# Optimization experiments

Measured on AMD Instinct MI355X. Metric: run time of the kernel, lower is better.

## Reference

```python
import jax, jax.numpy as jnp
import numpy as np

NUM_LEVELS = 4
RADIUS = 3
B, H, W, C = 2, 64, 64, 64
N = 4096


def _bilinear_sample(feat, coords):
    # feat: (B, H, W, C); coords: (B, N, 2) in [0,W-1]x[0,H-1]
    Bf, Hf, Wf, Cf = feat.shape
    x = coords[..., 0]
    y = coords[..., 1]
    x0 = jnp.clip(jnp.floor(x).astype(jnp.int32), 0, Wf - 1)
    x1 = jnp.clip(jnp.floor(x).astype(jnp.int32) + 1, 0, Wf - 1)
    y0 = jnp.clip(jnp.floor(y).astype(jnp.int32), 0, Hf - 1)
    y1 = jnp.clip(jnp.floor(y).astype(jnp.int32) + 1, 0, Hf - 1)
    # weights use the CLIPPED corner coords (matches original code order)
    wa = (x1.astype(jnp.float32) - x) * (y1.astype(jnp.float32) - y)
    wb = (x1.astype(jnp.float32) - x) * (y - y0.astype(jnp.float32))
    wc = (x - x0.astype(jnp.float32)) * (y1.astype(jnp.float32) - y)
    wd = (x - x0.astype(jnp.float32)) * (y - y0.astype(jnp.float32))
    bidx = jnp.arange(Bf)[:, None]
    Ia = feat[bidx, y0, x0, :]
    Ib = feat[bidx, y1, x0, :]
    Ic = feat[bidx, y0, x1, :]
    Id = feat[bidx, y1, x1, :]
    return (wa[..., None] * Ia + wb[..., None] * Ib
            + wc[..., None] * Ic + wd[..., None] * Id)


def _build_pyramid(fmap2):
    # pyramid holds L2-normalized fmap2 at successively halved resolutions
    f = fmap2 / (jnp.linalg.norm(fmap2, axis=-1, keepdims=True) + 1e-6)
    pyr = [f]
    cur = f
    for level in range(NUM_LEVELS - 1):
        cur = jax.image.resize(
            cur, (B, H // 2 ** (level + 1), W // 2 ** (level + 1), C),
            method='bilinear')
        pyr.append(cur)
    return pyr


def _corr_block(fmap1, fmap2, coords):
    r = RADIUS
    # fmap1 is normalized in the original but its result is unused; replicate faithfully
    _ = fmap1 / (jnp.linalg.norm(fmap1, axis=-1, keepdims=True) + 1e-6)
    pyramid = _build_pyramid(fmap2)
    # (dx, dy) offsets, dy outer / dx inner to match original concat order
    offsets = jnp.array([[dx, dy] for dy in range(-r, r + 1)
                         for dx in range(-r, r + 1)], dtype=jnp.float32)  # (K,2)
    K = offsets.shape[0]
    outs = []
    for level, corr in enumerate(pyramid):
        scale = 2 ** level
        H_l, W_l = corr.shape[1], corr.shape[2]
        coords_scaled = coords / scale                       # (B,N,2)
        coords_off = coords_scaled[None] + offsets[:, None, None, :]  # (K,B,N,2)
        coords_off = jnp.clip(coords_off,
                              jnp.array([0.0, 0.0]),
                              jnp.array([W_l - 1, H_l - 1], dtype=jnp.float32))
        sampled = jax.vmap(_bilinear_sample, in_axes=(None, 0))(corr, coords_off)  # (K,B,N,C)
        outs.append(jnp.moveaxis(sampled, 0, 2).reshape(coords.shape[0], coords.shape[1], K * corr.shape[-1]))
    return jnp.concatenate(outs, axis=-1)  # (B, N, NUM_LEVELS*K*C)


def setup_inputs() -> dict:
    key = jax.random.key(0)
    k1, k2, k3 = jax.random.split(key, 3)
    fmap1 = jax.random.normal(k1, (B, H, W, C), dtype=jnp.float32)
    fmap2 = jax.random.normal(k2, (B, H, W, C), dtype=jnp.float32)
    coords = jax.random.uniform(k3, (B, N, 2), dtype=jnp.float32) \
        * jnp.array([W - 1, H - 1], dtype=jnp.float32)
    return {"fmap1": fmap1, "fmap2": fmap2, "coords": coords}


def reference(fmap1, fmap2, coords):
    return _corr_block(fmap1, fmap2, coords)
```

## Files before the change

### kernel.cpp

```cpp
#include <hip/hip_runtime.h>
#include <math.h>


__global__ __launch_bounds__(256) void normalize_kernel(
    const float* __restrict__ in, float* __restrict__ out) {
  int gtid = blockIdx.x * 256 + threadIdx.x;
  int wave = gtid >> 6;
  int lane = gtid & 63;
  float v = in[wave * 64 + lane];
  float ss = v * v;
  #pragma unroll
  for (int m = 32; m >= 1; m >>= 1) ss += __shfl_xor(ss, m);
  out[wave * 64 + lane] = v / (sqrtf(ss) + 1e-6f);
}

__global__ __launch_bounds__(256) void downsample_kernel(
    const float* __restrict__ in, float* __restrict__ out, int Si) {
  int So = Si >> 1;
  int gtid = blockIdx.x * 256 + threadIdx.x;
  int wave = gtid >> 6;
  int lane = gtid & 63;
  int ox = wave % So;
  int t  = wave / So;
  int oy = t % So;
  int b  = t / So;

  int xs[4], ys[4];
  float wx[4], wy[4];
  float bw[4] = {0.25f, 0.75f, 0.75f, 0.25f};
  float sx = 0.f, sy = 0.f;
  #pragma unroll
  for (int tt = 0; tt < 4; tt++) {
    int jx = 2 * ox - 1 + tt;
    bool vx = (jx >= 0) && (jx < Si);
    xs[tt] = vx ? jx : 0;
    wx[tt] = vx ? bw[tt] : 0.f;
    sx += wx[tt];
    int jy = 2 * oy - 1 + tt;
    bool vy = (jy >= 0) && (jy < Si);
    ys[tt] = vy ? jy : 0;
    wy[tt] = vy ? bw[tt] : 0.f;
    sy += wy[tt];
  }
  float ix = 1.f / sx, iy = 1.f / sy;
  #pragma unroll
  for (int tt = 0; tt < 4; tt++) { wx[tt] *= ix; wy[tt] *= iy; }

  float acc = 0.f;
  #pragma unroll
  for (int a = 0; a < 4; a++) {
    const float* rp = in + ((long)(b * Si + ys[a]) * Si) * 64 + lane;
    float row = 0.f;
    #pragma unroll
    for (int tt = 0; tt < 4; tt++) row += wx[tt] * rp[xs[tt] * 64];
    acc += wy[a] * row;
  }
  out[((long)(b * So + oy) * So + ox) * 64 + lane] = acc;
}

__global__ __launch_bounds__(448, 4) void corr_sample_reg(
    const float* __restrict__ pyr, const float* __restrict__ coords,
    float* __restrict__ out) {
  unsigned bn = blockIdx.x;
  unsigned b = bn >> 12;
  int t = threadIdx.x;
  int c4 = t & 15;
  int g = t >> 4;
  int l = g / 7;
  int dyi = g - l * 7;

  int Wl = 64 >> l;
  float sc = 1.0f / (float)(1 << l);
  float fmx = (float)(Wl - 1);
  unsigned base4 = (524288u - (524288u >> (2 * l))) / 3u;

  float cx = coords[bn * 2 + 0];
  float cy = coords[bn * 2 + 1];
  float cxs = cx * sc, cys = cy * sc;

  float y = fminf(fmaxf(cys + (float)(dyi - 3), 0.f), fmx);
  int y0 = (int)floorf(y);
  int y1 = min(y0 + 1, Wl - 1);
  float wy0 = (float)y1 - y;
  float wy1 = y - (float)y0;

  const float4* p4 = (const float4*)pyr;
  unsigned pixb = (unsigned)(b * Wl * Wl);
  unsigned r0 = base4 + ((pixb + (unsigned)(y0 * Wl)) << 4) + (unsigned)c4;
  unsigned r1 = base4 + ((pixb + (unsigned)(y1 * Wl)) << 4) + (unsigned)c4;

  unsigned ob = bn * 3136u + (unsigned)l * 784u + ((unsigned)(dyi * 7) << 4) +
                (unsigned)c4;
  float4* o4 = (float4*)out;

  int px = -1;
  float4 a0 = make_float4(0.f, 0.f, 0.f, 0.f), a1 = a0;
  #pragma unroll
  for (int dxi = 0; dxi < 7; ++dxi) {
    float x = fminf(fmaxf(cxs + (float)(dxi - 3), 0.f), fmx);
    int x0 = (int)floorf(x);
    int x1 = min(x0 + 1, Wl - 1);
    float wx0 = (float)x1 - x;
    float wx1 = x - (float)x0;

    float4 b0, b1;
    if (x0 == px) {
      b0 = a0; b1 = a1;
    } else {
      b0 = p4[r0 + ((unsigned)x0 << 4)];
      b1 = p4[r1 + ((unsigned)x0 << 4)];
    }
    a0 = p4[r0 + ((unsigned)x1 << 4)];
    a1 = p4[r1 + ((unsigned)x1 << 4)];
    px = x1;

    float4 r;
    r.x = wx0 * (wy0 * b0.x + wy1 * b1.x) + wx1 * (wy0 * a0.x + wy1 * a1.x);
    r.y = wx0 * (wy0 * b0.y + wy1 * b1.y) + wx1 * (wy0 * a0.y + wy1 * a1.y);
    r.z = wx0 * (wy0 * b0.z + wy1 * b1.z) + wx1 * (wy0 * a0.z + wy1 * a1.z);
    r.w = wx0 * (wy0 * b0.w + wy1 * b1.w) + wx1 * (wy0 * a0.w + wy1 * a1.w);
    o4[ob + (unsigned)(dxi << 4)] = r;
  }
}

extern "C" void kernel_launch(void* const* d_in, const int* in_sizes, int n_in,
                              void* d_out, int out_size, void* d_ws, size_t ws_size,
                              hipStream_t stream) {
  const float* fmap2 = (const float*)d_in[1];
  const float* coords = (const float*)d_in[2];
  float* out = (float*)d_out;
  float* pyr = (float*)d_ws;

  normalize_kernel<<<2048, 256, 0, stream>>>(fmap2, pyr);
  downsample_kernel<<<512, 256, 0, stream>>>(pyr,          pyr + 524288, 64);
  downsample_kernel<<<128, 256, 0, stream>>>(pyr + 524288, pyr + 655360, 32);
  downsample_kernel<<< 32, 256, 0, stream>>>(pyr + 655360, pyr + 688128, 16);
  corr_sample_reg<<<8192, 448, 0, stream>>>(pyr, coords, out);
}
```

Baseline: 87.74 us.

## Fuse pyramid build into one persistent kernel with atomic grid barriers

Merges the normalize kernel and the three downsample kernels into a single 256-block kernel that uses atomic-counter grid barriers between levels, plus a memset to reset the counter. The aim is to cut the launch overhead and inter-kernel gaps of four small launches. It risks deadlock if not all blocks are co-resident, and it adds spin-wait and memset costs.

```diff
diff --git a/kernel.cpp b/kernel.cpp
--- a/kernel.cpp
+++ b/kernel.cpp
@@ -2,60 +2,85 @@
 #include <math.h>
 
 
-__global__ __launch_bounds__(256) void normalize_kernel(
-    const float* __restrict__ in, float* __restrict__ out) {
-  int gtid = blockIdx.x * 256 + threadIdx.x;
-  int wave = gtid >> 6;
-  int lane = gtid & 63;
-  float v = in[wave * 64 + lane];
-  float ss = v * v;
-  #pragma unroll
-  for (int m = 32; m >= 1; m >>= 1) ss += __shfl_xor(ss, m);
-  out[wave * 64 + lane] = v / (sqrtf(ss) + 1e-6f);
+#define NBLK 256
+
+__device__ __forceinline__ void gridbar(unsigned* __restrict__ cnt, unsigned k) {
+  __syncthreads();
+  if (threadIdx.x == 0) {
+    __hip_atomic_fetch_add(cnt, 1u, __ATOMIC_ACQ_REL, __HIP_MEMORY_SCOPE_AGENT);
+    while (__hip_atomic_load(cnt, __ATOMIC_ACQUIRE, __HIP_MEMORY_SCOPE_AGENT) <
+           k * (unsigned)NBLK)
+      __builtin_amdgcn_s_sleep(1);
+  }
+  __syncthreads();
+  __threadfence();
 }
 
-__global__ __launch_bounds__(256) void downsample_kernel(
-    const float* __restrict__ in, float* __restrict__ out, int Si) {
-  int So = Si >> 1;
-  int gtid = blockIdx.x * 256 + threadIdx.x;
-  int wave = gtid >> 6;
-  int lane = gtid & 63;
-  int ox = wave % So;
-  int t  = wave / So;
-  int oy = t % So;
-  int b  = t / So;
-
+__device__ __forceinline__ float ds_tap(const float* __restrict__ in, int Si,
+                                        int b, int oy, int ox, int lane) {
   int xs[4], ys[4];
   float wx[4], wy[4];
   float bw[4] = {0.25f, 0.75f, 0.75f, 0.25f};
   float sx = 0.f, sy = 0.f;
   #pragma unroll
-  for (int tt = 0; tt < 4; tt++) {
-    int jx = 2 * ox - 1 + tt;
+  for (int t = 0; t < 4; t++) {
+    int jx = 2 * ox - 1 + t;
     bool vx = (jx >= 0) && (jx < Si);
-    xs[tt] = vx ? jx : 0;
-    wx[tt] = vx ? bw[tt] : 0.f;
-    sx += wx[tt];
-    int jy = 2 * oy - 1 + tt;
+    xs[t] = vx ? jx : 0;
+    wx[t] = vx ? bw[t] : 0.f;
+    sx += wx[t];
+    int jy = 2 * oy - 1 + t;
     bool vy = (jy >= 0) && (jy < Si);
-    ys[tt] = vy ? jy : 0;
-    wy[tt] = vy ? bw[tt] : 0.f;
-    sy += wy[tt];
+    ys[t] = vy ? jy : 0;
+    wy[t] = vy ? bw[t] : 0.f;
+    sy += wy[t];
   }
   float ix = 1.f / sx, iy = 1.f / sy;
   #pragma unroll
-  for (int tt = 0; tt < 4; tt++) { wx[tt] *= ix; wy[tt] *= iy; }
-
+  for (int t = 0; t < 4; t++) { wx[t] *= ix; wy[t] *= iy; }
   float acc = 0.f;
   #pragma unroll
   for (int a = 0; a < 4; a++) {
-    const float* rp = in + ((long)(b * Si + ys[a]) * Si) * 64 + lane;
+    const float* rp = in + ((b * Si + ys[a]) * Si) * 64 + lane;
     float row = 0.f;
     #pragma unroll
-    for (int tt = 0; tt < 4; tt++) row += wx[tt] * rp[xs[tt] * 64];
+    for (int t = 0; t < 4; t++) row += wx[t] * rp[xs[t] * 64];
     acc += wy[a] * row;
   }
-  out[((long)(b * So + oy) * So + ox) * 64 + lane] = acc;
+  return acc;
+}
+
+__global__ __launch_bounds__(256) void pyramid_coop(
+    const float* __restrict__ raw, float* __restrict__ pyr,
+    unsigned* __restrict__ cnt) {
+  int lane = threadIdx.x & 63;
+  int gw = blockIdx.x * 4 + (threadIdx.x >> 6);
+
+  for (int w = gw; w < 8192; w += 4 * NBLK) {
+    float v = raw[w * 64 + lane];
+    float ss = v * v;
+    #pragma unroll
+    for (int m = 32; m >= 1; m >>= 1) ss += __shfl_xor(ss, m);
+    pyr[w * 64 + lane] = v / (sqrtf(ss) + 1e-6f);
+  }
+  gridbar(cnt, 1);
+
+  for (int p = gw; p < 2048; p += 4 * NBLK) {
+    int b = p >> 10, r = p & 1023, oy = r >> 5, ox = r & 31;
+    pyr[524288 + p * 64 + lane] = ds_tap(pyr, 64, b, oy, ox, lane);
+  }
+  gridbar(cnt, 2);
+
+  for (int p = gw; p < 512; p += 4 * NBLK) {
+    int b = p >> 8, r = p & 255, oy = r >> 4, ox = r & 15;
+    pyr[655360 + p * 64 + lane] = ds_tap(pyr + 524288, 32, b, oy, ox, lane);
+  }
+  gridbar(cnt, 3);
+
+  for (int p = gw; p < 128; p += 4 * NBLK) {
+    int b = p >> 6, r = p & 63, oy = r >> 3, ox = r & 7;
+    pyr[688128 + p * 64 + lane] = ds_tap(pyr + 655360, 16, b, oy, ox, lane);
+  }
 }
 
 __global__ __launch_bounds__(448, 4) void corr_sample_reg(
@@ -130,10 +155,9 @@
   const float* coords = (const float*)d_in[2];
   float* out = (float*)d_out;
   float* pyr = (float*)d_ws;
+  unsigned* cnt = (unsigned*)((char*)d_ws + 2785280);
 
-  normalize_kernel<<<2048, 256, 0, stream>>>(fmap2, pyr);
-  downsample_kernel<<<512, 256, 0, stream>>>(pyr,          pyr + 524288, 64);
-  downsample_kernel<<<128, 256, 0, stream>>>(pyr + 524288, pyr + 655360, 32);
-  downsample_kernel<<< 32, 256, 0, stream>>>(pyr + 655360, pyr + 688128, 16);
+  hipMemsetAsync(cnt, 0, 64, stream);
+  pyramid_coop<<<NBLK, 256, 0, stream>>>(fmap2, pyr, cnt);
   corr_sample_reg<<<8192, 448, 0, stream>>>(pyr, coords, out);
 }
```

New measurement: 179.9 us. 105% more time.
